# Kernel tuning notes

Hardware: AMD Instinct MI355X
Metric: run time of the kernel (lower is better)

Reference implementation:

```python
import jax, jax.numpy as jnp
import numpy as np
from jax import lax

B, C, L, H = 32, 256, 1280, 5
D = L // H  # head dim = 256
EPS = 1e-5


def setup_inputs() -> dict:
    key = jax.random.key(0)
    ks = jax.random.split(key, 16)
    s = 0.02
    inp = {
        "x": jax.random.normal(ks[0], (B, C, L), jnp.float32),
        # rank encoder Linear(L, L)
        "re_w": jax.random.normal(ks[1], (L, L), jnp.float32) * s,
        "re_b": jnp.zeros((L,), jnp.float32),
        # layer norms
        "ln1_g": jnp.ones((L,), jnp.float32), "ln1_b": jnp.zeros((L,), jnp.float32),
        "ln2_g": jnp.ones((L,), jnp.float32), "ln2_b": jnp.zeros((L,), jnp.float32),
        # attention projections (stored [in, out]; y @ W + b)
        "wq": jax.random.normal(ks[2], (L, L), jnp.float32) * s, "bq": jnp.zeros((L,), jnp.float32),
        "wk": jax.random.normal(ks[3], (L, L), jnp.float32) * s, "bk": jnp.zeros((L,), jnp.float32),
        "wv": jax.random.normal(ks[4], (L, L), jnp.float32) * s, "bv": jnp.zeros((L,), jnp.float32),
        "wo": jax.random.normal(ks[5], (L, L), jnp.float32) * s, "bo": jnp.zeros((L,), jnp.float32),
        # FFN (ffn_size == hidden_size == L in this module)
        "ffn_w1": jax.random.normal(ks[6], (L, L), jnp.float32) * s, "ffn_b1": jnp.zeros((L,), jnp.float32),
        "ffn_w2": jax.random.normal(ks[7], (L, L), jnp.float32) * s, "ffn_b2": jnp.zeros((L,), jnp.float32),
        # Conv1d(C, C, k=3, stride=1, pad=1, bias=False) + BatchNorm1d (eval) + ReLU
        "conv_w": jax.random.normal(ks[8], (C, C, 3), jnp.float32) * (2.0 / (C * 3)) ** 0.5,
        "bn_g": jnp.ones((C,), jnp.float32), "bn_b": jnp.zeros((C,), jnp.float32),
        "bn_m": jnp.zeros((C,), jnp.float32), "bn_v": jnp.ones((C,), jnp.float32),
    }
    return inp


def _layernorm(t, g, b):
    m = jnp.mean(t, axis=-1, keepdims=True)
    v = jnp.var(t, axis=-1, keepdims=True)
    return (t - m) * lax.rsqrt(v + EPS) * g + b


def reference(x, re_w, re_b, ln1_g, ln1_b, ln2_g, ln2_b,
              wq, bq, wk, bk, wv, bv, wo, bo,
              ffn_w1, ffn_b1, ffn_w2, ffn_b2,
              conv_w, bn_g, bn_b, bn_m, bn_v):
    b_, c_, l_ = x.shape
    # _getrank_: rank from double argsort (descending), mapped to (L - rank)/L
    rank_i = jnp.argsort(jnp.argsort(-x, axis=-1), axis=-1)
    rank = (l_ - rank_i).astype(x.dtype) / l_
    node = x + rank @ re_w + re_b                      # [B, C, L]

    # EncoderLayer: pre-LN MHSA (attn_bias is None in this call path)
    y = _layernorm(node, ln1_g, ln1_b)
    scale = D ** -0.5
    q = (y @ wq + bq).reshape(b_, c_, H, D).transpose(0, 2, 1, 3) * scale  # [B,H,C,D]
    k = (y @ wk + bk).reshape(b_, c_, H, D).transpose(0, 2, 1, 3)
    v = (y @ wv + bv).reshape(b_, c_, H, D).transpose(0, 2, 1, 3)
    attn = jax.nn.softmax(jnp.einsum('bhqd,bhkd->bhqk', q, k), axis=-1)   # [B,H,C,C]
    o = jnp.einsum('bhqk,bhkd->bhqd', attn, v)
    o = o.transpose(0, 2, 1, 3).reshape(b_, c_, l_) @ wo + bo
    h = node + o  # dropout is identity in eval

    # FFN sublayer
    y2 = _layernorm(h, ln2_g, ln2_b)
    f = jax.nn.gelu(y2 @ ffn_w1 + ffn_b1, approximate=False) @ ffn_w2 + ffn_b2
    h = h + f                                           # [B, C, L]

    # ConvBNRelu: Conv1d(k=3, s=1, p=1, no bias) -> BN (eval stats) -> ReLU
    conv = lax.conv_general_dilated(h, conv_w, window_strides=(1,),
                                    padding=[(1, 1)],
                                    dimension_numbers=('NCH', 'OIH', 'NCH'))
    bn = (conv - bn_m[None, :, None]) * lax.rsqrt(bn_v[None, :, None] + EPS)
    bn = bn * bn_g[None, :, None] + bn_b[None, :, None]
    return jax.nn.relu(bn)
```

## Files before the change

### kernel.cpp

```cpp
#include <hip/hip_runtime.h>
#include <hip/hip_bf16.h>
#include <stdint.h>

#define L_   1280
#define B_   32
#define C_   256
#define H_   5
#define D_   256
#define BC_  8192
#define EPSV 1e-5f

typedef __attribute__((ext_vector_type(8))) short bf16x8;
typedef __attribute__((ext_vector_type(4))) float f32x4;
typedef __hip_bfloat16 bf16;

__device__ __forceinline__ bf16 f2bf(float v) { return __float2bfloat16(v); }
__device__ __forceinline__ float bf2f(bf16 v) { return __bfloat162float(v); }

#define GLDS16(gptr, lptr)                                                        \
    __builtin_amdgcn_global_load_lds(                                             \
        (const __attribute__((address_space(1))) void*)(gptr),                    \
        (__attribute__((address_space(3))) void*)(lptr), 16, 0, 0)

struct WtArgs { const float* src[7]; bf16* dst[7]; };

__global__ __launch_bounds__(256) void transpose7(WtArgs a) {
    const int mat = blockIdx.z;
    const float* src = a.src[mat];
    bf16* dst = a.dst[mat];
    __shared__ float tile[32][33];
    const int bx = blockIdx.x * 32;
    const int by = blockIdx.y * 32;
    const int tx = threadIdx.x, ty = threadIdx.y;
    #pragma unroll
    for (int r = ty; r < 32; r += 8)
        tile[r][tx] = src[(size_t)(by + r) * L_ + bx + tx];
    __syncthreads();
    #pragma unroll
    for (int r = ty; r < 32; r += 8)
        dst[(size_t)(bx + r) * L_ + by + tx] = f2bf(tile[tx][r]);
}

__global__ __launch_bounds__(256) void prep_conv(const float* cw, const float* g, const float* b,
                                                 const float* m, const float* v,
                                                 bf16* WT, float* sc, float* bi) {
    const int i = blockIdx.x * 256 + threadIdx.x;
    if (i < 3 * 256 * 256) {
        const int co = i / 768;
        const int r = i - co * 768;
        const int t = r >> 8, ci = r & 255;
        WT[i] = f2bf(cw[(co * 256 + ci) * 3 + t]);
    }
    if (i < 256) {
        const float s = g[i] * rsqrtf(v[i] + EPSV);
        sc[i] = s;
        bi[i] = b[i] - m[i] * s;
    }
}

__global__ __launch_bounds__(256) void rank_kernel(const float* __restrict__ x, bf16* __restrict__ R) {
    __shared__ float vals[L_];
    __shared__ float sv[L_];
    __shared__ int hist[256];
    __shared__ int pfx[256];
    __shared__ int cur[256];
    const int row = blockIdx.x, tid = threadIdx.x;
    const float* src = x + (size_t)row * L_;
    for (int i = tid; i < L_; i += 256) vals[i] = src[i];
    hist[tid] = 0;
    __syncthreads();
    float myv[5]; int myb[5];
    #pragma unroll
    for (int ii = 0; ii < 5; ii++) {
        const float v = vals[tid + ii * 256];
        int bk = (int)((4.0f - v) * 32.0f);
        bk = bk < 0 ? 0 : (bk > 255 ? 255 : bk);
        myv[ii] = v; myb[ii] = bk;
        atomicAdd(&hist[bk], 1);
    }
    __syncthreads();
    pfx[tid] = hist[tid];
    __syncthreads();
    for (int off = 1; off < 256; off <<= 1) {
        int t = (tid >= off) ? pfx[tid - off] : 0;
        __syncthreads();
        pfx[tid] += t;
        __syncthreads();
    }
    cur[tid] = pfx[tid] - hist[tid];
    __syncthreads();
    #pragma unroll
    for (int ii = 0; ii < 5; ii++) {
        const int pos = atomicAdd(&cur[myb[ii]], 1);
        sv[pos] = myv[ii];
    }
    __syncthreads();
    #pragma unroll
    for (int ii = 0; ii < 5; ii++) {
        const int bk = myb[ii]; const float v = myv[ii];
        const int s = pfx[bk] - hist[bk], e = pfx[bk];
        int cg = s;
        for (int p = s; p < e; p++) cg += (sv[p] > v) ? 1 : 0;
        R[(size_t)row * L_ + tid + ii * 256] = f2bf((float)(L_ - cg) * (1.0f / L_));
    }
}

__global__ __launch_bounds__(256) void ln_kernel(const bf16* __restrict__ in,
                                                 const float* __restrict__ g,
                                                 const float* __restrict__ b,
                                                 bf16* __restrict__ out) {
    const int row = blockIdx.x, tid = threadIdx.x;
    const bf16* src = in + (size_t)row * L_;
    uint2 ra = ((const uint2*)src)[tid];
    bf16 a4[4]; *(uint2*)a4 = ra;
    const float a0 = bf2f(a4[0]), a1 = bf2f(a4[1]), a2 = bf2f(a4[2]), a3 = bf2f(a4[3]);
    float s = a0 + a1 + a2 + a3;
    float ss = a0 * a0 + a1 * a1 + a2 * a2 + a3 * a3;
    float b0 = 0, b1 = 0, b2 = 0, b3 = 0;
    if (tid < 64) {
        uint2 rb = ((const uint2*)src)[256 + tid];
        bf16 b4[4]; *(uint2*)b4 = rb;
        b0 = bf2f(b4[0]); b1 = bf2f(b4[1]); b2 = bf2f(b4[2]); b3 = bf2f(b4[3]);
        s += b0 + b1 + b2 + b3;
        ss += b0 * b0 + b1 * b1 + b2 * b2 + b3 * b3;
    }
    #pragma unroll
    for (int off = 32; off > 0; off >>= 1) {
        s += __shfl_down(s, off, 64);
        ss += __shfl_down(ss, off, 64);
    }
    __shared__ float rs[4], rss[4];
    __shared__ float mean_s, rstd_s;
    if ((tid & 63) == 0) { rs[tid >> 6] = s; rss[tid >> 6] = ss; }
    __syncthreads();
    if (tid == 0) {
        const float S = rs[0] + rs[1] + rs[2] + rs[3];
        const float SS = rss[0] + rss[1] + rss[2] + rss[3];
        const float m = S * (1.0f / L_);
        const float var = SS * (1.0f / L_) - m * m;
        mean_s = m; rstd_s = rsqrtf(var + EPSV);
    }
    __syncthreads();
    const float m = mean_s, r = rstd_s;
    {
        const int c = tid * 4;
        bf16 t4[4];
        t4[0] = f2bf((a0 - m) * r * g[c + 0] + b[c + 0]);
        t4[1] = f2bf((a1 - m) * r * g[c + 1] + b[c + 1]);
        t4[2] = f2bf((a2 - m) * r * g[c + 2] + b[c + 2]);
        t4[3] = f2bf((a3 - m) * r * g[c + 3] + b[c + 3]);
        *(uint2*)(out + (size_t)row * L_ + c) = *(uint2*)t4;
    }
    if (tid < 64) {
        const int c = 1024 + tid * 4;
        bf16 t4[4];
        t4[0] = f2bf((b0 - m) * r * g[c + 0] + b[c + 0]);
        t4[1] = f2bf((b1 - m) * r * g[c + 1] + b[c + 1]);
        t4[2] = f2bf((b2 - m) * r * g[c + 2] + b[c + 2]);
        t4[3] = f2bf((b3 - m) * r * g[c + 3] + b[c + 3]);
        *(uint2*)(out + (size_t)row * L_ + c) = *(uint2*)t4;
    }
}

__global__ __launch_bounds__(256) void softmax_kernel(const bf16* __restrict__ S, bf16* __restrict__ P) {
    const int row = blockIdx.x * 4 + (threadIdx.x >> 6);
    const int l = threadIdx.x & 63;
    const bf16* src = S + (size_t)row * 256 + l * 4;
    uint2 raw = *(const uint2*)src;
    bf16 s4[4]; *(uint2*)s4 = raw;
    float v0 = bf2f(s4[0]), v1 = bf2f(s4[1]);
    float v2 = bf2f(s4[2]), v3 = bf2f(s4[3]);
    float mx = fmaxf(fmaxf(v0, v1), fmaxf(v2, v3));
    #pragma unroll
    for (int off = 1; off < 64; off <<= 1) mx = fmaxf(mx, __shfl_xor(mx, off, 64));
    const float e0 = expf(v0 - mx), e1 = expf(v1 - mx), e2 = expf(v2 - mx), e3 = expf(v3 - mx);
    float sm = e0 + e1 + e2 + e3;
    #pragma unroll
    for (int off = 1; off < 64; off <<= 1) sm += __shfl_xor(sm, off, 64);
    const float inv = 1.0f / sm;
    bf16 t4[4] = { f2bf(e0 * inv), f2bf(e1 * inv), f2bf(e2 * inv), f2bf(e3 * inv) };
    *(uint2*)(P + (size_t)row * 256 + l * 4) = *(uint2*)t4;
}

__global__ __launch_bounds__(256) void zero_pads(bf16* h2T) {
    const int i = blockIdx.x * 256 + threadIdx.x;
    const int b = i >> 9;
    const int which = (i >> 8) & 1;
    const int ci = i & 255;
    const long row = which ? 1281 : 0;
    h2T[(long)b * (1282 * 256) + row * 256 + ci] = f2bf(0.0f);
}

struct GemmP {
    const bf16* A;  long lda, sA1, sA2;
    const bf16* Bt; long ldb, sB1, sB2;
    int zmod;
    int K;
    float* outF; bf16* outB; bf16* outB2; bf16* outB3; long ldc, sC1, sC2;
    const float* bias; const float* bias2; const float* bias3;
    const float* res; const bf16* resB; long ldres, sR1, sR2;
    const float* rowscale; const float* rowbias;
    float scale;
};

constexpr int E_NODE = 0;
constexpr int E_HRES = 1;
constexpr int E_BF16 = 5;
constexpr int E_GELU = 6;
constexpr int E_FFN2T = 7;
constexpr int E_CONVBNR = 8;
constexpr int E_QKV = 9;

template <int EPI, int BM>
__global__ __launch_bounds__(256) void gemm_bt(GemmP p) {
    constexpr int MREP  = BM / 32;
    constexpr int WM    = BM / 2;
    constexpr int ABUF  = BM * 32;
    constexpr int BBASE = 3 * ABUF;

    const int nwg  = gridDim.x * gridDim.y * gridDim.z;
    const int orig = (blockIdx.z * gridDim.y + blockIdx.y) * gridDim.x + blockIdx.x;
    int bx, rowg;
    if ((nwg & 7) == 0) {
        const int chunk = nwg >> 3;
        const int xcd = orig & 7, pos = orig >> 3;
        const int rpc = chunk / gridDim.x;
        if (rpc * gridDim.x == chunk) {
            bx   = pos / rpc;
            rowg = xcd * rpc + (pos - bx * rpc);
        } else {
            const int wgid = xcd * chunk + pos;
            bx = wgid % gridDim.x; rowg = wgid / gridDim.x;
        }
    } else {
        bx = blockIdx.x; rowg = blockIdx.z * gridDim.y + blockIdx.y;
    }
    const int by = rowg % gridDim.y;
    const int bz = rowg / gridDim.y;

    const int zq = bz / p.zmod, zr = bz % p.zmod;
    const bf16* A  = p.A  + (long)zq * p.sA1 + (long)zr * p.sA2;
    const bf16* Bt = p.Bt + (long)zq * p.sB1 + (long)zr * p.sB2;
    const int row0 = by * BM, col0 = bx * 128;

    __shared__ __align__(16) bf16 shm[3 * (BM * 32) + 12288];

    const int tid = threadIdx.x;
    const int l = tid & 63, w = tid >> 6;
    const int wr = w >> 1, wc = w & 1;

    f32x4 acc[MREP][4];
    #pragma unroll
    for (int m = 0; m < MREP; m++)
        #pragma unroll
        for (int n = 0; n < 4; n++)
            acc[m][n] = (f32x4){0.f, 0.f, 0.f, 0.f};

    const bf16* gA = A  + (long)(row0 + w * 16 + (l >> 2)) * p.lda + (l & 3) * 8;
    const bf16* gB = Bt + (long)(col0 + w * 16 + (l >> 2)) * p.ldb + (l & 3) * 8;

    auto STAGE = [&](int buf) {
        bf16* lA = shm + buf * ABUF;
        bf16* lB = shm + BBASE + buf * 4096;
        #pragma unroll
        for (int r = 0; r < BM / 64; r++)
            GLDS16(gA + (long)r * 64 * p.lda, lA + r * 2048 + w * 512);
        GLDS16(gB,               lB + w * 512);
        GLDS16(gB + 64 * p.ldb,  lB + 2048 + w * 512);
        gA += 32; gB += 32;
    };
    auto COMPUTE = [&](int buf) {
        const bf16* lA = shm + buf * ABUF;
        const bf16* lB = shm + BBASE + buf * 4096;
        bf16x8 aF[MREP], bF[4];
        #pragma unroll
        for (int m = 0; m < MREP; m++)
            aF[m] = *(const bf16x8*)(lA + (wr * WM + m * 16 + (l & 15)) * 32 + (l >> 4) * 8);
        #pragma unroll
        for (int n = 0; n < 4; n++)
            bF[n] = *(const bf16x8*)(lB + (wc * 64 + n * 16 + (l & 15)) * 32 + (l >> 4) * 8);
        #pragma unroll
        for (int m = 0; m < MREP; m++)
            #pragma unroll
            for (int n = 0; n < 4; n++)
                acc[m][n] = __builtin_amdgcn_mfma_f32_16x16x32_bf16(aF[m], bF[n], acc[m][n], 0, 0, 0);
    };

    const int nt = p.K >> 5;
    STAGE(0); STAGE(1);
    int cb = 0, sb = 2;
    for (int t = 0; t < nt - 1; ++t) {
        if constexpr (BM == 256)
            asm volatile("s_waitcnt vmcnt(6)" ::: "memory");
        else
            asm volatile("s_waitcnt vmcnt(4)" ::: "memory");
        __builtin_amdgcn_sched_barrier(0);
        __builtin_amdgcn_s_barrier();
        if (t + 2 < nt) STAGE(sb);
        COMPUTE(cb);
        cb = (cb == 2) ? 0 : cb + 1;
        sb = (sb == 2) ? 0 : sb + 1;
    }
    asm volatile("s_waitcnt vmcnt(0)" ::: "memory");
    __builtin_amdgcn_sched_barrier(0);
    __builtin_amdgcn_s_barrier();
    COMPUTE(cb);

    const long cz = (long)zq * p.sC1 + (long)zr * p.sC2;
    const long rz = (long)zq * p.sR1 + (long)zr * p.sR2;
    #pragma unroll
    for (int m = 0; m < MREP; m++) {
        #pragma unroll
        for (int n = 0; n < 4; n++) {
            const int gcol = col0 + wc * 64 + n * 16 + (l & 15);
            if constexpr (EPI == E_QKV) {
                if (gcol >= 2560) {
                    const int c3 = gcol - 2560;
                    const int h_ = c3 >> 8, d_ = c3 & 255;
                    const int gr0 = row0 + wr * WM + m * 16 + (l >> 4) * 4;
                    const int b_ = gr0 >> 8, c0b = gr0 & 255;
                    const float bb = p.bias3[c3];
                    bf16 t4[4];
                    #pragma unroll
                    for (int j = 0; j < 4; j++) t4[j] = f2bf(acc[m][n][j] + bb);
                    *(uint2*)(p.outB3 + (((long)((b_ * H_ + h_) * 256 + d_)) << 8) + c0b) =
                        *(uint2*)t4;
                    continue;
                }
            }
            #pragma unroll
            for (int j = 0; j < 4; j++) {
                const int grow = row0 + wr * WM + m * 16 + (l >> 4) * 4 + j;
                const float v = acc[m][n][j];
                if constexpr (EPI == E_NODE) {
                    p.outB[cz + (long)grow * p.ldc + gcol] =
                        f2bf(v + p.bias[gcol] + p.res[rz + (long)grow * p.ldres + gcol]);
                } else if constexpr (EPI == E_HRES) {
                    p.outB[cz + (long)grow * p.ldc + gcol] =
                        f2bf(v + p.bias[gcol] + bf2f(p.resB[rz + (long)grow * p.ldres + gcol]));
                } else if constexpr (EPI == E_BF16) {
                    p.outB[cz + (long)grow * p.ldc + gcol] = f2bf(v);
                } else if constexpr (EPI == E_GELU) {
                    const float t = v + p.bias[gcol];
                    p.outB[cz + (long)grow * p.ldc + gcol] =
                        f2bf(0.5f * t * (1.0f + erff(t * 0.70710678f)));
                } else if constexpr (EPI == E_FFN2T) {
                    const float t = v + p.bias[gcol] +
                                    bf2f(p.resB[rz + (long)grow * p.ldres + gcol]);
                    const int b_ = grow >> 8, ci = grow & 255;
                    p.outB[(long)b_ * (1282 * 256) + (long)(gcol + 1) * 256 + ci] = f2bf(t);
                } else if constexpr (EPI == E_CONVBNR) {
                    const float t = v * p.rowscale[grow] + p.rowbias[grow];
                    p.outF[cz + (long)grow * p.ldc + gcol] = fmaxf(t, 0.0f);
                } else if constexpr (EPI == E_QKV) {
                    if (gcol < 1280) {
                        p.outB[(long)grow * L_ + gcol] = f2bf((v + p.bias[gcol]) * p.scale);
                    } else {
                        const int c2 = gcol - 1280;
                        p.outB2[(long)grow * L_ + c2] = f2bf(v + p.bias2[c2]);
                    }
                }
            }
        }
    }
}

extern "C" void kernel_launch(void* const* d_in, const int* in_sizes, int n_in,
                              void* d_out, int out_size, void* d_ws, size_t ws_size,
                              hipStream_t stream) {
    const float* x    = (const float*)d_in[0];
    const float* re_w = (const float*)d_in[1];
    const float* re_b = (const float*)d_in[2];
    const float* ln1g = (const float*)d_in[3];
    const float* ln1b = (const float*)d_in[4];
    const float* ln2g = (const float*)d_in[5];
    const float* ln2b = (const float*)d_in[6];
    const float* wq   = (const float*)d_in[7];
    const float* bq   = (const float*)d_in[8];
    const float* wk   = (const float*)d_in[9];
    const float* bk   = (const float*)d_in[10];
    const float* wv   = (const float*)d_in[11];
    const float* bv   = (const float*)d_in[12];
    const float* wo   = (const float*)d_in[13];
    const float* bo   = (const float*)d_in[14];
    const float* fw1  = (const float*)d_in[15];
    const float* fb1  = (const float*)d_in[16];
    const float* fw2  = (const float*)d_in[17];
    const float* fb2  = (const float*)d_in[18];
    const float* convw = (const float*)d_in[19];
    const float* bng  = (const float*)d_in[20];
    const float* bnb  = (const float*)d_in[21];
    const float* bnm  = (const float*)d_in[22];
    const float* bnv  = (const float*)d_in[23];
    float* out = (float*)d_out;

    char* ws = (char*)d_ws;
    const size_t SZ_WT     = (size_t)L_ * L_ * 2;
    const size_t SZ_ACT_BF = (size_t)BC_ * L_ * 2;
    const size_t SZ_H2T    = (size_t)B_ * 1282 * 256 * 2;
    const size_t SZ_S      = (size_t)160 * 256 * 256 * 4;

    size_t off = 0;
    bf16* Wt[7];
    for (int i = 0; i < 7; i++) { Wt[i] = (bf16*)(ws + off); off += SZ_WT; }
    bf16* WconvT   = (bf16*)(ws + off); off += 393216;
    float* bnscale = (float*)(ws + off); off += 1024;
    float* bnbias  = (float*)(ws + off); off += 1024;
    bf16* RP  = (bf16*)(ws + off); off += SZ_ACT_BF;
    bf16* Yb  = (bf16*)(ws + off); off += SZ_ACT_BF;
    bf16* Qb  = (bf16*)(ws + off); off += SZ_ACT_BF;
    bf16* Kb  = (bf16*)(ws + off); off += SZ_H2T;
    float* Sb = (float*)(ws + off); off += SZ_S;
    bf16* nodeB = (bf16*)(ws + off); off += SZ_ACT_BF;
    bf16* Sbf = (bf16*)Sb;
    bf16* VT  = Sbf + (size_t)160 * 65536;
    (void)in_sizes; (void)n_in; (void)out_size;

    if (ws_size < off) return;

    WtArgs wa;
    wa.src[0] = re_w; wa.src[1] = wq; wa.src[2] = wk; wa.src[3] = wv;
    wa.src[4] = wo;  wa.src[5] = fw1; wa.src[6] = fw2;
    for (int i = 0; i < 7; i++) wa.dst[i] = Wt[i];
    transpose7<<<dim3(40, 40, 7), dim3(32, 8), 0, stream>>>(wa);
    prep_conv<<<dim3(768), 256, 0, stream>>>(convw, bng, bnb, bnm, bnv, WconvT, bnscale, bnbias);

    rank_kernel<<<dim3(BC_), 256, 0, stream>>>(x, RP);

    const dim3 gBig(L_ / 128, BC_ / 128, 1);
    const dim3 gQKV(3840 / 128, BC_ / 256, 1);
    const dim3 gAttn(2, 2, 160);
    const dim3 blk(256);

    {
        GemmP p{}; p.zmod = 1; p.K = L_;
        p.A = RP; p.lda = L_; p.Bt = Wt[0]; p.ldb = L_;
        p.outB = nodeB; p.ldc = L_; p.bias = re_b; p.res = x; p.ldres = L_;
        gemm_bt<E_NODE, 128><<<gBig, blk, 0, stream>>>(p);
    }
    ln_kernel<<<dim3(BC_), blk, 0, stream>>>(nodeB, ln1g, ln1b, Yb);
    {
        GemmP p{}; p.zmod = 1; p.K = L_;
        p.A = Yb; p.lda = L_; p.Bt = Wt[1]; p.ldb = L_;
        p.outB = Qb; p.outB2 = Kb; p.outB3 = VT;
        p.bias = bq; p.bias2 = bk; p.bias3 = bv; p.scale = 0.0625f;
        gemm_bt<E_QKV, 256><<<gQKV, blk, 0, stream>>>(p);
    }
    {
        GemmP p{}; p.zmod = H_; p.K = 256;
        p.A = Qb;  p.lda = L_; p.sA1 = (long)C_ * L_; p.sA2 = 256;
        p.Bt = Kb; p.ldb = L_; p.sB1 = (long)C_ * L_; p.sB2 = 256;
        p.outB = Sbf; p.ldc = 256; p.sC1 = (long)H_ * 65536; p.sC2 = 65536;
        gemm_bt<E_BF16, 128><<<gAttn, blk, 0, stream>>>(p);
    }
    softmax_kernel<<<dim3(160 * 256 / 4), blk, 0, stream>>>(Sbf, RP);
    {
        GemmP p{}; p.zmod = H_; p.K = 256;
        p.A = RP;  p.lda = 256; p.sA1 = (long)H_ * 65536; p.sA2 = 65536;
        p.Bt = VT; p.ldb = 256; p.sB1 = (long)H_ * 65536; p.sB2 = 65536;
        p.outB = Qb; p.ldc = L_; p.sC1 = (long)C_ * L_; p.sC2 = 256;
        gemm_bt<E_BF16, 128><<<gAttn, blk, 0, stream>>>(p);
    }
    {
        GemmP p{}; p.zmod = 1; p.K = L_;
        p.A = Qb; p.lda = L_; p.Bt = Wt[4]; p.ldb = L_;
        p.outB = nodeB; p.ldc = L_; p.bias = bo; p.resB = nodeB; p.ldres = L_;
        gemm_bt<E_HRES, 128><<<gBig, blk, 0, stream>>>(p);
    }
    ln_kernel<<<dim3(BC_), blk, 0, stream>>>(nodeB, ln2g, ln2b, RP);
    {
        GemmP p{}; p.zmod = 1; p.K = L_;
        p.A = RP; p.lda = L_; p.Bt = Wt[5]; p.ldb = L_;
        p.outB = Yb; p.ldc = L_; p.bias = fb1;
        gemm_bt<E_GELU, 128><<<gBig, blk, 0, stream>>>(p);
    }
    zero_pads<<<dim3(64), blk, 0, stream>>>(Kb);
    {
        GemmP p{}; p.zmod = 1; p.K = L_;
        p.A = Yb; p.lda = L_; p.Bt = Wt[6]; p.ldb = L_;
        p.outB = Kb; p.bias = fb2; p.resB = nodeB; p.ldres = L_;
        gemm_bt<E_FFN2T, 128><<<gBig, blk, 0, stream>>>(p);
    }
    {
        GemmP p{}; p.zmod = 1; p.K = 768;
        p.A = WconvT; p.lda = 768;
        p.Bt = Kb; p.ldb = 256; p.sB1 = 1282 * 256;
        p.outF = out; p.ldc = L_; p.sC1 = (long)C_ * L_;
        p.rowscale = bnscale; p.rowbias = bnbias;
        gemm_bt<E_CONVBNR, 128><<<dim3(L_ / 128, 2, B_), blk, 0, stream>>>(p);
    }
}
```

Before: 517.3 us.

## Split GEMM main loop into two interleaved halves with staged loads and setprio

Restructures the bf16 GEMM main loop so each k-step is split into two phases: the A-tile prefetch is issued after the first half of LDS fragment reads, and the B-tile prefetch after the second. Each phase runs half of the MFMAs at raised wave priority, with an extra workgroup barrier between halves. The aim is to interleave global-to-LDS traffic with MFMA issue and reduce contention between waves. The extra barrier per iteration adds synchronisation cost, and the vmcnt wait counts still assume the old issue order.

```diff
diff --git a/kernel.cpp b/kernel.cpp
--- a/kernel.cpp
+++ b/kernel.cpp
@@ -214,6 +214,7 @@
 template <int EPI, int BM>
 __global__ __launch_bounds__(256) void gemm_bt(GemmP p) {
     constexpr int MREP  = BM / 32;
+    constexpr int HREP  = MREP / 2;
     constexpr int WM    = BM / 2;
     constexpr int ABUF  = BM * 32;
     constexpr int BBASE = 3 * ABUF;
@@ -259,35 +260,23 @@
     const bf16* gA = A  + (long)(row0 + w * 16 + (l >> 2)) * p.lda + (l & 3) * 8;
     const bf16* gB = Bt + (long)(col0 + w * 16 + (l >> 2)) * p.ldb + (l & 3) * 8;
 
-    auto STAGE = [&](int buf) {
+    auto STAGE_A = [&](int buf) {
         bf16* lA = shm + buf * ABUF;
-        bf16* lB = shm + BBASE + buf * 4096;
         #pragma unroll
         for (int r = 0; r < BM / 64; r++)
             GLDS16(gA + (long)r * 64 * p.lda, lA + r * 2048 + w * 512);
+        gA += 32;
+    };
+    auto STAGE_B = [&](int buf) {
+        bf16* lB = shm + BBASE + buf * 4096;
         GLDS16(gB,               lB + w * 512);
         GLDS16(gB + 64 * p.ldb,  lB + 2048 + w * 512);
-        gA += 32; gB += 32;
+        gB += 32;
     };
-    auto COMPUTE = [&](int buf) {
-        const bf16* lA = shm + buf * ABUF;
-        const bf16* lB = shm + BBASE + buf * 4096;
-        bf16x8 aF[MREP], bF[4];
-        #pragma unroll
-        for (int m = 0; m < MREP; m++)
-            aF[m] = *(const bf16x8*)(lA + (wr * WM + m * 16 + (l & 15)) * 32 + (l >> 4) * 8);
-        #pragma unroll
-        for (int n = 0; n < 4; n++)
-            bF[n] = *(const bf16x8*)(lB + (wc * 64 + n * 16 + (l & 15)) * 32 + (l >> 4) * 8);
-        #pragma unroll
-        for (int m = 0; m < MREP; m++)
-            #pragma unroll
-            for (int n = 0; n < 4; n++)
-                acc[m][n] = __builtin_amdgcn_mfma_f32_16x16x32_bf16(aF[m], bF[n], acc[m][n], 0, 0, 0);
-    };
 
     const int nt = p.K >> 5;
-    STAGE(0); STAGE(1);
+    STAGE_A(0); STAGE_B(0);
+    STAGE_A(1); STAGE_B(1);
     int cb = 0, sb = 2;
     for (int t = 0; t < nt - 1; ++t) {
         if constexpr (BM == 256)
@@ -296,15 +285,64 @@
             asm volatile("s_waitcnt vmcnt(4)" ::: "memory");
         __builtin_amdgcn_sched_barrier(0);
         __builtin_amdgcn_s_barrier();
-        if (t + 2 < nt) STAGE(sb);
-        COMPUTE(cb);
+        __builtin_amdgcn_sched_barrier(0);
+
+        const bf16* lA = shm + cb * ABUF;
+        const bf16* lB = shm + BBASE + cb * 4096;
+        const bool doStage = (t + 2 < nt);
+
+        bf16x8 aF[MREP], bF[4];
+        #pragma unroll
+        for (int n = 0; n < 4; n++)
+            bF[n] = *(const bf16x8*)(lB + (wc * 64 + n * 16 + (l & 15)) * 32 + (l >> 4) * 8);
+        #pragma unroll
+        for (int m = 0; m < HREP; m++)
+            aF[m] = *(const bf16x8*)(lA + (wr * WM + m * 16 + (l & 15)) * 32 + (l >> 4) * 8);
+        if (doStage) STAGE_A(sb);
+        __builtin_amdgcn_s_setprio(1);
+        #pragma unroll
+        for (int m = 0; m < HREP; m++)
+            #pragma unroll
+            for (int n = 0; n < 4; n++)
+                acc[m][n] = __builtin_amdgcn_mfma_f32_16x16x32_bf16(aF[m], bF[n], acc[m][n], 0, 0, 0);
+        __builtin_amdgcn_s_setprio(0);
+        __builtin_amdgcn_s_barrier();
+        __builtin_amdgcn_sched_barrier(0);
+
+        #pragma unroll
+        for (int m = HREP; m < MREP; m++)
+            aF[m] = *(const bf16x8*)(lA + (wr * WM + m * 16 + (l & 15)) * 32 + (l >> 4) * 8);
+        if (doStage) STAGE_B(sb);
+        __builtin_amdgcn_s_setprio(1);
+        #pragma unroll
+        for (int m = HREP; m < MREP; m++)
+            #pragma unroll
+            for (int n = 0; n < 4; n++)
+                acc[m][n] = __builtin_amdgcn_mfma_f32_16x16x32_bf16(aF[m], bF[n], acc[m][n], 0, 0, 0);
+        __builtin_amdgcn_s_setprio(0);
+
         cb = (cb == 2) ? 0 : cb + 1;
         sb = (sb == 2) ? 0 : sb + 1;
     }
     asm volatile("s_waitcnt vmcnt(0)" ::: "memory");
     __builtin_amdgcn_sched_barrier(0);
     __builtin_amdgcn_s_barrier();
-    COMPUTE(cb);
+    {
+        const bf16* lA = shm + cb * ABUF;
+        const bf16* lB = shm + BBASE + cb * 4096;
+        bf16x8 aF[MREP], bF[4];
+        #pragma unroll
+        for (int n = 0; n < 4; n++)
+            bF[n] = *(const bf16x8*)(lB + (wc * 64 + n * 16 + (l & 15)) * 32 + (l >> 4) * 8);
+        #pragma unroll
+        for (int m = 0; m < MREP; m++)
+            aF[m] = *(const bf16x8*)(lA + (wr * WM + m * 16 + (l & 15)) * 32 + (l >> 4) * 8);
+        #pragma unroll
+        for (int m = 0; m < MREP; m++)
+            #pragma unroll
+            for (int n = 0; n < 4; n++)
+                acc[m][n] = __builtin_amdgcn_mfma_f32_16x16x32_bf16(aF[m], bF[n], acc[m][n], 0, 0, 0);
+    }
 
     const long cz = (long)zq * p.sC1 + (long)zr * p.sC2;
     const long rz = (long)zq * p.sR1 + (long)zr * p.sR2;
```

Result: no change. 514.4 us (-0.6%).
